# Kernel optimization log

Hardware: AMD Instinct MI355X
Metric: run time of the kernel (lower is better)

The kernel has to match this reference:

```python
import jax, jax.numpy as jnp
import numpy as np

N, E, IN, ED, HID, B, K = 50000, 800000, 128, 64, 256, 128, 1000


def setup_inputs() -> dict:
    key = jax.random.key(0)
    ks = jax.random.split(key, 16)

    def lin(k, fi, fo):
        k1, k2 = jax.random.split(k)
        s = 1.0 / np.sqrt(fi)
        return (jax.random.uniform(k1, (fi, fo), jnp.float32, -s, s),
                jax.random.uniform(k2, (fo,), jnp.float32, -s, s))

    We, be = lin(ks[0], ED, IN)        # GINEConv edge projection edge_dim -> in_channels
    W1, b1 = lin(ks[1], IN, HID)       # GINE nn layer 1
    W2, b2 = lin(ks[2], HID, HID)      # GINE nn layer 2
    Wg1, bg1 = lin(ks[3], HID, 128)    # gate_nn layer 1
    Wg2, bg2 = lin(ks[4], 128, 1)      # gate_nn layer 2
    Wh, bh = lin(ks[5], HID, K)        # head

    x = jax.random.normal(ks[6], (N, IN), jnp.float32)
    edge_index = jax.random.randint(ks[7], (2, E), 0, N, jnp.int64)
    edge_attr = jax.random.normal(ks[8], (E, ED), jnp.float32)
    batch = jnp.sort(jax.random.randint(ks[9], (N,), 0, B, jnp.int64))

    return {"x": x, "edge_index": edge_index, "edge_attr": edge_attr, "batch": batch,
            "We": We, "be": be, "W1": W1, "b1": b1, "W2": W2, "b2": b2,
            "Wg1": Wg1, "bg1": bg1, "Wg2": Wg2, "bg2": bg2, "Wh": Wh, "bh": bh}


def reference(x, edge_index, edge_attr, batch, We, be, W1, b1, W2, b2,
              Wg1, bg1, Wg2, bg2, Wh, bh):
    src, dst = edge_index[0], edge_index[1]
    # GINEConv message: ReLU(x_j + Lin(edge_attr)), scatter-add to dst (eps=0)
    e = edge_attr @ We + be                      # [E, IN]
    m = jax.nn.relu(x[src] + e)                  # [E, IN]
    agg = jax.ops.segment_sum(m, dst, num_segments=N)  # [N, IN]
    h = x + agg                                  # (1+eps)*x + agg, eps=0
    h = jax.nn.relu(h @ W1 + b1) @ W2 + b2       # [N, HID]
    # GlobalAttention: segment softmax of gate over graphs, weighted sum
    gate = jax.nn.relu(h @ Wg1 + bg1) @ Wg2 + bg2            # [N, 1]
    gmax = jax.ops.segment_max(gate, batch, num_segments=B)  # [B, 1]
    a = jnp.exp(gate - gmax[batch])
    denom = jax.ops.segment_sum(a, batch, num_segments=B)    # [B, 1]
    attn = a / denom[batch]
    pooled = jax.ops.segment_sum(attn * h, batch, num_segments=B)  # [B, HID]
    logits = pooled @ Wh + bh                    # [B, K]
    return (logits, pooled)
```

## Files before the change

kernel.cpp:

```cpp
#include <hip/hip_runtime.h>
#include <stdint.h>

#define NN    50000
#define EE    800000
#define IN_C  128
#define ED_C  64
#define HID_C 256
#define BB    128
#define KK    1000
#define G1_C  128
#define NV    50176


typedef __attribute__((ext_vector_type(8))) short bfrag;
typedef __attribute__((ext_vector_type(4))) float f4acc;

__device__ __forceinline__ unsigned short f2bs(float f){
  unsigned u = __float_as_uint(f);
  return (unsigned short)((u + 0x7fffu + ((u >> 16) & 1u)) >> 16);
}
__device__ __forceinline__ float bs2f(unsigned short s){
  return __uint_as_float(((unsigned)s) << 16);
}

__device__ __forceinline__ void atomicMaxFloat(float* addr, float val){
  int old = __float_as_int(*addr);
  while (__int_as_float(old) < val){
    int assumed = old;
    old = atomicCAS((int*)addr, assumed, __float_as_int(val));
    if (old == assumed) break;
  }
}

__global__ __launch_bounds__(256) void k_setup(
    const float* __restrict__ We, const float* __restrict__ W1,
    const float* __restrict__ W2, const float* __restrict__ Wg1,
    const float* __restrict__ x,
    unsigned short* __restrict__ Wet, unsigned short* __restrict__ W1t,
    unsigned short* __restrict__ W2t, unsigned short* __restrict__ Wg1t,
    unsigned short* __restrict__ xb,
    float* __restrict__ agg, int* __restrict__ cnt, int* __restrict__ fill,
    int* __restrict__ aux, float* __restrict__ gmax, float* __restrict__ denom,
    float* __restrict__ pooled)
{
  size_t i = (size_t)blockIdx.x * 256 + threadIdx.x;
  if (i < 128 * 64){ int c = (int)i >> 6, k = (int)i & 63;  Wet[i]  = f2bs(We[k * 128 + c]); }
  if (i < 256 * 128){ int n = (int)i >> 7, k = (int)i & 127; W1t[i]  = f2bs(W1[k * 256 + n]); }
  if (i < 256 * 256){ int n = (int)i >> 8, k = (int)i & 255; W2t[i]  = f2bs(W2[k * 256 + n]); }
  if (i < 128 * 256){ int n = (int)i >> 8, k = (int)i & 255; Wg1t[i] = f2bs(Wg1[k * 128 + n]); }
  if (i < (size_t)NN * IN_C / 4){
    const float4 v = ((const float4*)x)[i];
    ushort4 o;
    o.x = f2bs(v.x); o.y = f2bs(v.y); o.z = f2bs(v.z); o.w = f2bs(v.w);
    ((ushort4*)xb)[i] = o;
  }
  if (i < (size_t)NN * IN_C) agg[i] = 0.f;
  if (i < NV){ cnt[i] = 0; fill[i] = 0; }
  if (i < 256) aux[i] = 0;
  if (i < BB){ gmax[i] = -1e30f; denom[i] = 0.f; }
  if (i < BB * HID_C) pooled[i] = 0.f;
}

__global__ __launch_bounds__(256) void k_hist(const int* __restrict__ ei,
                                              int* __restrict__ cnt){
  int e = blockIdx.x * 256 + threadIdx.x;
  if (e < EE) atomicAdd(&cnt[ei[EE + e]], 1);
}

__global__ __launch_bounds__(256) void k_scan1(const int* __restrict__ cnt,
                                               int* __restrict__ off,
                                               int* __restrict__ aux){
  __shared__ int s[256];
  int t = threadIdx.x, i = blockIdx.x * 256 + t;
  int val = cnt[i];
  s[t] = val; __syncthreads();
#pragma unroll
  for (int o = 1; o < 256; o <<= 1){
    int v = (t >= o) ? s[t - o] : 0;
    __syncthreads();
    s[t] += v;
    __syncthreads();
  }
  off[i] = s[t] - val;
  if (t == 255) aux[blockIdx.x] = s[255];
}

__global__ __launch_bounds__(256) void k_scan2(int* __restrict__ aux){
  __shared__ int s[256];
  int t = threadIdx.x;
  int val = aux[t];
  s[t] = val; __syncthreads();
#pragma unroll
  for (int o = 1; o < 256; o <<= 1){
    int v = (t >= o) ? s[t - o] : 0;
    __syncthreads();
    s[t] += v;
    __syncthreads();
  }
  aux[t] = s[t] - val;
}

__global__ __launch_bounds__(256) void k_scan3(int* __restrict__ off,
                                               const int* __restrict__ aux){
  int i = blockIdx.x * 256 + threadIdx.x;
  off[i] += aux[blockIdx.x];
}

__global__ __launch_bounds__(256) void k_scatter(const int* __restrict__ ei,
                                                 const int* __restrict__ off,
                                                 int* __restrict__ fill,
                                                 uint4* __restrict__ sorted){
  int e = blockIdx.x * 256 + threadIdx.x;
  if (e < EE){
    int s = ei[e], d = ei[EE + e];
    int pos = off[d] + atomicAdd(&fill[d], 1);
    sorted[pos] = make_uint4((unsigned)e, (unsigned)s, (unsigned)d, 0u);
  }
}

__global__ __launch_bounds__(256, 4) void k_edge2(
    const unsigned short* __restrict__ xb, const uint4* __restrict__ sorted,
    const float* __restrict__ edge_attr,
    const unsigned short* __restrict__ Wet, const float* __restrict__ be,
    float* __restrict__ agg)
{
  __shared__ float msgS[64 * 132];
  __shared__ uint4 sE[64];
  __shared__ int runStart[66];
  __shared__ int nRunsS;
  unsigned short* eaS = (unsigned short*)msgS;

  const int tid = threadIdx.x;
  const int e0 = blockIdx.x * 64;
  if (tid < 64) sE[tid] = sorted[e0 + tid];
  __syncthreads();

  const int lane = tid & 63, wv = tid >> 6;
  const int q = lane >> 4, l15 = lane & 15;
  const int g0 = wv * 16;

  const int xrow = g0 + (lane >> 2);
  const int xc0 = (lane & 3) * 32;
  const unsigned short* xptr = xb + (size_t)((int)sE[xrow].y) * IN_C + xc0;
  uint4 xr[4];
#pragma unroll
  for (int j = 0; j < 4; ++j) xr[j] = *(const uint4*)(xptr + j * 8);

#pragma unroll
  for (int t = 0; t < 4; ++t){
    int f4 = t * 256 + tid;
    int er = f4 >> 4;
    int kk = (f4 & 15) * 4;
    int eid = (int)sE[er].x;
    const float4 v = *(const float4*)(edge_attr + (size_t)eid * ED_C + kk);
    unsigned p0 = (unsigned)f2bs(v.x) | ((unsigned)f2bs(v.y) << 16);
    unsigned p1 = (unsigned)f2bs(v.z) | ((unsigned)f2bs(v.w) << 16);
    *(uint2*)&eaS[er * 72 + kk] = make_uint2(p0, p1);
  }

  if (tid < 64){
    bool flag = (tid == 0) || ((int)sE[tid].z != (int)sE[tid - 1].z);
    unsigned long long m = __ballot(flag);
    int pre = __popcll(m & ((1ull << tid) - 1ull));
    if ((m >> tid) & 1ull) runStart[pre] = tid;
    if (tid == 0){
      int nr = __popcll(m);
      nRunsS = nr;
      runStart[nr] = 64;
    }
  }
  __syncthreads();

  f4acc acc[8];
  const f4acc zz = {0.f, 0.f, 0.f, 0.f};
#pragma unroll
  for (int nt = 0; nt < 8; ++nt) acc[nt] = zz;

#pragma unroll
  for (int ks = 0; ks < 2; ++ks){
    bfrag a = *(const bfrag*)&eaS[(g0 + l15) * 72 + ks * 32 + q * 8];
#pragma unroll
    for (int nt = 0; nt < 8; ++nt){
      int c = nt * 16 + l15;
      bfrag b = *(const bfrag*)(Wet + c * ED_C + ks * 32 + q * 8);
      acc[nt] = __builtin_amdgcn_mfma_f32_16x16x32_bf16(a, b, acc[nt], 0, 0, 0);
    }
  }

  float bev[8];
#pragma unroll
  for (int nt = 0; nt < 8; ++nt) bev[nt] = be[nt * 16 + l15];

  __syncthreads();

#pragma unroll
  for (int nt = 0; nt < 8; ++nt){
    int c = nt * 16 + l15;
#pragma unroll
    for (int r = 0; r < 4; ++r)
      msgS[(g0 + q * 4 + r) * 132 + c] = acc[nt][r] + bev[nt];
  }

  {
    float* mr = &msgS[xrow * 132 + xc0];
#pragma unroll
    for (int jj = 0; jj < 4; ++jj){
      const uint4 u = xr[jj];
      float4 w0 = *(float4*)(mr + jj * 8);
      float4 w1 = *(float4*)(mr + jj * 8 + 4);
      w0.x = fmaxf(w0.x + __uint_as_float(u.x << 16), 0.f);
      w0.y = fmaxf(w0.y + __uint_as_float(u.x & 0xffff0000u), 0.f);
      w0.z = fmaxf(w0.z + __uint_as_float(u.y << 16), 0.f);
      w0.w = fmaxf(w0.w + __uint_as_float(u.y & 0xffff0000u), 0.f);
      w1.x = fmaxf(w1.x + __uint_as_float(u.z << 16), 0.f);
      w1.y = fmaxf(w1.y + __uint_as_float(u.z & 0xffff0000u), 0.f);
      w1.z = fmaxf(w1.z + __uint_as_float(u.w << 16), 0.f);
      w1.w = fmaxf(w1.w + __uint_as_float(u.w & 0xffff0000u), 0.f);
      *(float4*)(mr + jj * 8) = w0;
      *(float4*)(mr + jj * 8 + 4) = w1;
    }
  }
  __syncthreads();

  {
    const int col = tid & 127;
    const int h = tid >> 7;
    const int nR = nRunsS;
    for (int i = h; i < nR; i += 2){
      int s = runStart[i], e = runStart[i + 1];
      int dst = (int)sE[s].z;
      float run = 0.f;
      for (int r = s; r < e; ++r) run += msgS[r * 132 + col];
      size_t a = (size_t)dst * IN_C + col;
      if (s == 0 || e == 64) atomicAdd(&agg[a], run);
      else                   agg[a] = run;
    }
  }
}

__global__ __launch_bounds__(256) void k_h0(const float* __restrict__ agg,
                                            const float* __restrict__ x,
                                            unsigned short* __restrict__ h0b){
  int i = blockIdx.x * 256 + threadIdx.x;
  if (i < NN * IN_C) h0b[i] = f2bs(agg[i] + x[i]);
}

template<int K, bool RELU, bool OB16, bool GATE>
__global__ __launch_bounds__(256) void k_gemm(
    const unsigned short* __restrict__ A, const unsigned short* __restrict__ Wt,
    const float* __restrict__ bias, unsigned short* __restrict__ outb,
    int M, int Ntot,
    const float* __restrict__ Wg2, const float* __restrict__ bg2,
    float* __restrict__ gateOut)
{
  __shared__ unsigned short aS[64 * 40];
  __shared__ unsigned short bS[128 * 40];
  __shared__ float gred[2][64];
  const int tid = threadIdx.x;
  const int lane = tid & 63, wv = tid >> 6;
  const int wi = wv >> 1, wj = wv & 1;
  const int q = lane >> 4, l15 = lane & 15;
  const int mb0 = blockIdx.x * 64;
  const int nb0 = blockIdx.y * 128;
  const int arow = tid >> 2, achk = tid & 3;

  f4acc acc[2][4];
  const f4acc zz = {0.f, 0.f, 0.f, 0.f};
#pragma unroll
  for (int mt = 0; mt < 2; ++mt)
#pragma unroll
    for (int nt = 0; nt < 4; ++nt) acc[mt][nt] = zz;

  for (int ks = 0; ks < K / 32; ++ks){
    {
      int m = mb0 + arow; if (m >= M) m = M - 1;
      const uint4 v = *(const uint4*)(A + (size_t)m * K + ks * 32 + achk * 8);
      *(uint4*)&aS[arow * 40 + achk * 8] = v;
    }
#pragma unroll
    for (int i = 0; i < 2; ++i){
      int idx = i * 256 + tid;
      int row = idx >> 2, chk = idx & 3;
      const uint4 v = *(const uint4*)(Wt + (size_t)(nb0 + row) * K + ks * 32 + chk * 8);
      *(uint4*)&bS[row * 40 + chk * 8] = v;
    }
    __syncthreads();
    bfrag a[2], b[4];
#pragma unroll
    for (int mt = 0; mt < 2; ++mt)
      a[mt] = *(const bfrag*)&aS[(wi * 32 + mt * 16 + l15) * 40 + q * 8];
#pragma unroll
    for (int nt = 0; nt < 4; ++nt)
      b[nt] = *(const bfrag*)&bS[(wj * 64 + nt * 16 + l15) * 40 + q * 8];
#pragma unroll
    for (int mt = 0; mt < 2; ++mt)
#pragma unroll
      for (int nt = 0; nt < 4; ++nt)
        acc[mt][nt] = __builtin_amdgcn_mfma_f32_16x16x32_bf16(a[mt], b[nt], acc[mt][nt], 0, 0, 0);
    __syncthreads();
  }

  const int mb = mb0 + wi * 32;
  const int nb = nb0 + wj * 64;

  if (GATE){
    float wg2v[4];
#pragma unroll
    for (int nt = 0; nt < 4; ++nt) wg2v[nt] = Wg2[wj * 64 + nt * 16 + l15];
    float pr[2][4];
#pragma unroll
    for (int mt = 0; mt < 2; ++mt)
#pragma unroll
      for (int r = 0; r < 4; ++r) pr[mt][r] = 0.f;
#pragma unroll
    for (int nt = 0; nt < 4; ++nt){
      float bv = bias[wj * 64 + nt * 16 + l15];
#pragma unroll
      for (int mt = 0; mt < 2; ++mt)
#pragma unroll
        for (int r = 0; r < 4; ++r){
          float v = acc[mt][nt][r] + bv;
          v = v > 0.f ? v : 0.f;
          pr[mt][r] = fmaf(v, wg2v[nt], pr[mt][r]);
        }
    }
#pragma unroll
    for (int off = 1; off < 16; off <<= 1)
#pragma unroll
      for (int mt = 0; mt < 2; ++mt)
#pragma unroll
        for (int r = 0; r < 4; ++r)
          pr[mt][r] += __shfl_xor(pr[mt][r], off);
    if (l15 == 0){
#pragma unroll
      for (int mt = 0; mt < 2; ++mt)
#pragma unroll
        for (int r = 0; r < 4; ++r)
          gred[wj][wi * 32 + mt * 16 + q * 4 + r] = pr[mt][r];
    }
    __syncthreads();
    if (tid < 64){
      int m = mb0 + tid;
      if (m < M) gateOut[m] = gred[0][tid] + gred[1][tid] + bg2[0];
    }
  } else {
#pragma unroll
    for (int nt = 0; nt < 4; ++nt){
      int c = nb + nt * 16 + l15;
      float bv = bias[c];
#pragma unroll
      for (int mt = 0; mt < 2; ++mt){
#pragma unroll
        for (int r = 0; r < 4; ++r){
          int m = mb + mt * 16 + q * 4 + r;
          if (m < M){
            float v = acc[mt][nt][r] + bv;
            if (RELU) v = v > 0.f ? v : 0.f;
            if (OB16) outb[(size_t)m * Ntot + c] = f2bs(v);
          }
        }
      }
    }
  }
}

__global__ __launch_bounds__(256) void k_gmax(const float* __restrict__ gate,
                                              const int* __restrict__ batch,
                                              float* __restrict__ gmax, int nrows){
  __shared__ float wred[4];
  const int tid = threadIdx.x;
  const int n0 = blockIdx.x * 256;
  const int n = n0 + tid;
  const int nlast = (n0 + 255 < nrows) ? n0 + 255 : nrows - 1;
  const int bmin = batch[n0], bmax = batch[nlast];
  const int lane = tid & 63, wv = tid >> 6;
  float val = -3e38f; int b = bmax;
  if (n < nrows){ b = batch[n]; val = gate[n]; }
  for (int bb = bmin; bb <= bmax; ++bb){
    float v = (b == bb) ? val : -3e38f;
#pragma unroll
    for (int off = 1; off < 64; off <<= 1) v = fmaxf(v, __shfl_xor(v, off));
    if (lane == 0) wred[wv] = v;
    __syncthreads();
    if (tid == 0){
      float m = fmaxf(fmaxf(wred[0], wred[1]), fmaxf(wred[2], wred[3]));
      if (m > -1e37f) atomicMaxFloat(&gmax[bb], m);
    }
    __syncthreads();
  }
}

__global__ __launch_bounds__(256) void k_expsum(const float* __restrict__ gate,
                                                const int* __restrict__ batch,
                                                const float* __restrict__ gmax,
                                                float* __restrict__ aexp,
                                                float* __restrict__ denom, int nrows){
  __shared__ float wred[4];
  const int tid = threadIdx.x;
  const int n0 = blockIdx.x * 256;
  const int n = n0 + tid;
  const int nlast = (n0 + 255 < nrows) ? n0 + 255 : nrows - 1;
  const int bmin = batch[n0], bmax = batch[nlast];
  const int lane = tid & 63, wv = tid >> 6;
  float val = 0.f; int b = bmax;
  if (n < nrows){
    b = batch[n];
    val = expf(gate[n] - gmax[b]);
    aexp[n] = val;
  }
  for (int bb = bmin; bb <= bmax; ++bb){
    float v = (b == bb) ? val : 0.f;
#pragma unroll
    for (int off = 1; off < 64; off <<= 1) v += __shfl_xor(v, off);
    if (lane == 0) wred[wv] = v;
    __syncthreads();
    if (tid == 0){
      float s = wred[0] + wred[1] + wred[2] + wred[3];
      if (s != 0.f) atomicAdd(&denom[bb], s);
    }
    __syncthreads();
  }
}

__global__ __launch_bounds__(256) void k_pool(const unsigned short* __restrict__ h2b,
                                              const float* __restrict__ aexp,
                                              const float* __restrict__ denom,
                                              const int* __restrict__ batch,
                                              float* __restrict__ pooled, int nrows){
  const int c = threadIdx.x;
  const int n0 = blockIdx.x * 32;
  int n1 = n0 + 32; if (n1 > nrows) n1 = nrows;
  if (n0 >= nrows) return;
  float acc = 0.f;
  int curb = batch[n0];
  for (int n = n0; n < n1; ++n){
    int b = batch[n];
    if (b != curb){
      atomicAdd(&pooled[(size_t)curb * HID_C + c], acc);
      acc = 0.f; curb = b;
    }
    float wgt = aexp[n] / denom[b];
    acc = fmaf(wgt, bs2f(h2b[(size_t)n * HID_C + c]), acc);
  }
  atomicAdd(&pooled[(size_t)curb * HID_C + c], acc);
}

__global__ __launch_bounds__(256) void k_head(const float* __restrict__ pooled,
                                              const float* __restrict__ Wh,
                                              const float* __restrict__ bh,
                                              float* __restrict__ out_logits,
                                              float* __restrict__ out_pooled){
  __shared__ float p[HID_C];
  const int b = blockIdx.x, t = threadIdx.x;
  float pv = pooled[(size_t)b * HID_C + t];
  p[t] = pv;
  out_pooled[(size_t)b * HID_C + t] = pv;
  __syncthreads();
  for (int c = t; c < KK; c += 256){
    float acc = bh[c];
#pragma unroll 8
    for (int k = 0; k < HID_C; ++k)
      acc = fmaf(p[k], Wh[k * KK + c], acc);
    out_logits[(size_t)b * KK + c] = acc;
  }
}

extern "C" void kernel_launch(void* const* d_in, const int* in_sizes, int n_in,
                              void* d_out, int out_size, void* d_ws, size_t ws_size,
                              hipStream_t stream) {
  const float* x   = (const float*)d_in[0];
  const int*   ei  = (const int*)d_in[1];
  const float* ea  = (const float*)d_in[2];
  const int*   batch = (const int*)d_in[3];
  const float* We  = (const float*)d_in[4];
  const float* be  = (const float*)d_in[5];
  const float* W1  = (const float*)d_in[6];
  const float* b1  = (const float*)d_in[7];
  const float* W2  = (const float*)d_in[8];
  const float* b2  = (const float*)d_in[9];
  const float* Wg1 = (const float*)d_in[10];
  const float* bg1 = (const float*)d_in[11];
  const float* Wg2 = (const float*)d_in[12];
  const float* bg2 = (const float*)d_in[13];
  const float* Wh  = (const float*)d_in[14];
  const float* bh  = (const float*)d_in[15];

  float* out_logits = (float*)d_out;
  float* out_pooled = out_logits + (size_t)BB * KK;

  float* agg    = (float*)d_ws;
  float* gate   = agg   + (size_t)NN * IN_C;
  float* aexp   = gate  + NN;
  float* gmax   = aexp  + NN;
  float* denom  = gmax  + BB;
  float* pooled = denom + BB;
  float* fend   = pooled + (size_t)BB * HID_C;
  unsigned short* h0b  = (unsigned short*)fend;
  unsigned short* h1b  = h0b + (size_t)NN * IN_C;
  unsigned short* h2b  = h1b + (size_t)NN * HID_C;
  unsigned short* Wet  = h2b + (size_t)NN * HID_C;
  unsigned short* W1t  = Wet + 128 * 64;
  unsigned short* W2t  = W1t + 256 * 128;
  unsigned short* Wg1t = W2t + 256 * 256;
  unsigned short* xb   = Wg1t + 128 * 256;
  uint4* sorted = (uint4*)h1b;
  int* cnt  = (int*)(sorted + EE);
  int* off  = cnt + NV;
  int* fill = off + NV;
  int* aux  = fill + NV;

  k_setup<<<(NN * IN_C + 255) / 256, 256, 0, stream>>>(
      We, W1, W2, Wg1, x, Wet, W1t, W2t, Wg1t, xb,
      agg, cnt, fill, aux, gmax, denom, pooled);
  k_hist   <<<(EE + 255) / 256, 256, 0, stream>>>(ei, cnt);
  k_scan1  <<<NV / 256, 256, 0, stream>>>(cnt, off, aux);
  k_scan2  <<<1, 256, 0, stream>>>(aux);
  k_scan3  <<<NV / 256, 256, 0, stream>>>(off, aux);
  k_scatter<<<(EE + 255) / 256, 256, 0, stream>>>(ei, off, fill, sorted);
  k_edge2<<<EE / 64, 256, 0, stream>>>(xb, sorted, ea, Wet, be, agg);
  k_h0<<<(NN * IN_C + 255) / 256, 256, 0, stream>>>(agg, x, h0b);
  k_gemm<128, true,  true,  false><<<dim3(782, 2), 256, 0, stream>>>(
      h0b, W1t, b1, h1b, NN, HID_C, (const float*)0, (const float*)0, (float*)0);
  k_gemm<256, false, true,  false><<<dim3(782, 2), 256, 0, stream>>>(
      h1b, W2t, b2, h2b, NN, HID_C, (const float*)0, (const float*)0, (float*)0);
  k_gemm<256, true,  false, true ><<<dim3(782, 1), 256, 0, stream>>>(
      h2b, Wg1t, bg1, (unsigned short*)0, NN, G1_C, Wg2, bg2, gate);
  k_gmax  <<<(NN + 255) / 256, 256, 0, stream>>>(gate, batch, gmax, NN);
  k_expsum<<<(NN + 255) / 256, 256, 0, stream>>>(gate, batch, gmax, aexp, denom, NN);
  k_pool  <<<(NN + 31) / 32, 256, 0, stream>>>(h2b, aexp, denom, batch, pooled, NN);
  k_head<<<BB, 256, 0, stream>>>(pooled, Wh, bh, out_logits, out_pooled);
}
```

Baseline: 666.9 us.

## Fuse h0 into first GEMM, merge attention pooling and head, trim scans

Removes the k_h0 pass by having the first GEMM load fp32 agg and x, add them and convert to bf16 while staging the A tile. Replaces the gmax/expsum/pool/head kernels with one kernel per graph that binary-searches its node range in the sorted batch array. That kernel computes max, softmax denominator, pooled features and logits with no global atomics. It also folds the scan3 pass into scatter by adding the block offset there, and reuses the cnt array as the fill counter by zeroing it inside scan1. The trade-off is that the fused attention stage runs on only 128 blocks, each walking about 390 nodes serially, and the first GEMM now reads fp32 A, which is twice as many bytes, for each N-tile.

```diff
diff --git a/kernel.cpp b/kernel.cpp
--- a/kernel.cpp
+++ b/kernel.cpp
@@ -23,15 +23,6 @@
   return __uint_as_float(((unsigned)s) << 16);
 }
 
-__device__ __forceinline__ void atomicMaxFloat(float* addr, float val){
-  int old = __float_as_int(*addr);
-  while (__int_as_float(old) < val){
-    int assumed = old;
-    old = atomicCAS((int*)addr, assumed, __float_as_int(val));
-    if (old == assumed) break;
-  }
-}
-
 __global__ __launch_bounds__(256) void k_setup(
     const float* __restrict__ We, const float* __restrict__ W1,
     const float* __restrict__ W2, const float* __restrict__ Wg1,
@@ -39,9 +30,7 @@
     unsigned short* __restrict__ Wet, unsigned short* __restrict__ W1t,
     unsigned short* __restrict__ W2t, unsigned short* __restrict__ Wg1t,
     unsigned short* __restrict__ xb,
-    float* __restrict__ agg, int* __restrict__ cnt, int* __restrict__ fill,
-    int* __restrict__ aux, float* __restrict__ gmax, float* __restrict__ denom,
-    float* __restrict__ pooled)
+    float* __restrict__ agg, int* __restrict__ cnt, int* __restrict__ aux)
 {
   size_t i = (size_t)blockIdx.x * 256 + threadIdx.x;
   if (i < 128 * 64){ int c = (int)i >> 6, k = (int)i & 63;  Wet[i]  = f2bs(We[k * 128 + c]); }
@@ -55,10 +44,8 @@
     ((ushort4*)xb)[i] = o;
   }
   if (i < (size_t)NN * IN_C) agg[i] = 0.f;
-  if (i < NV){ cnt[i] = 0; fill[i] = 0; }
+  if (i < NV) cnt[i] = 0;
   if (i < 256) aux[i] = 0;
-  if (i < BB){ gmax[i] = -1e30f; denom[i] = 0.f; }
-  if (i < BB * HID_C) pooled[i] = 0.f;
 }
 
 __global__ __launch_bounds__(256) void k_hist(const int* __restrict__ ei,
@@ -67,7 +54,7 @@
   if (e < EE) atomicAdd(&cnt[ei[EE + e]], 1);
 }
 
-__global__ __launch_bounds__(256) void k_scan1(const int* __restrict__ cnt,
+__global__ __launch_bounds__(256) void k_scan1(int* __restrict__ cnt,
                                                int* __restrict__ off,
                                                int* __restrict__ aux){
   __shared__ int s[256];
@@ -82,6 +69,7 @@
     __syncthreads();
   }
   off[i] = s[t] - val;
+  cnt[i] = 0;
   if (t == 255) aux[blockIdx.x] = s[255];
 }
 
@@ -100,20 +88,15 @@
   aux[t] = s[t] - val;
 }
 
-__global__ __launch_bounds__(256) void k_scan3(int* __restrict__ off,
-                                               const int* __restrict__ aux){
-  int i = blockIdx.x * 256 + threadIdx.x;
-  off[i] += aux[blockIdx.x];
-}
-
 __global__ __launch_bounds__(256) void k_scatter(const int* __restrict__ ei,
                                                  const int* __restrict__ off,
+                                                 const int* __restrict__ aux,
                                                  int* __restrict__ fill,
                                                  uint4* __restrict__ sorted){
   int e = blockIdx.x * 256 + threadIdx.x;
   if (e < EE){
     int s = ei[e], d = ei[EE + e];
-    int pos = off[d] + atomicAdd(&fill[d], 1);
+    int pos = off[d] + aux[d >> 8] + atomicAdd(&fill[d], 1);
     sorted[pos] = make_uint4((unsigned)e, (unsigned)s, (unsigned)d, 0u);
   }
 }
@@ -238,16 +221,11 @@
   }
 }
 
-__global__ __launch_bounds__(256) void k_h0(const float* __restrict__ agg,
-                                            const float* __restrict__ x,
-                                            unsigned short* __restrict__ h0b){
-  int i = blockIdx.x * 256 + threadIdx.x;
-  if (i < NN * IN_C) h0b[i] = f2bs(agg[i] + x[i]);
-}
-
-template<int K, bool RELU, bool OB16, bool GATE>
+template<int K, bool RELU, bool OB16, bool GATE, bool AF>
 __global__ __launch_bounds__(256) void k_gemm(
-    const unsigned short* __restrict__ A, const unsigned short* __restrict__ Wt,
+    const unsigned short* __restrict__ A,
+    const float* __restrict__ aggA, const float* __restrict__ xA,
+    const unsigned short* __restrict__ Wt,
     const float* __restrict__ bias, unsigned short* __restrict__ outb,
     int M, int Ntot,
     const float* __restrict__ Wg2, const float* __restrict__ bg2,
@@ -274,8 +252,23 @@
   for (int ks = 0; ks < K / 32; ++ks){
     {
       int m = mb0 + arow; if (m >= M) m = M - 1;
-      const uint4 v = *(const uint4*)(A + (size_t)m * K + ks * 32 + achk * 8);
-      *(uint4*)&aS[arow * 40 + achk * 8] = v;
+      if (AF){
+        size_t base = (size_t)m * K + ks * 32 + achk * 8;
+        const float4 a0 = *(const float4*)(aggA + base);
+        const float4 a1 = *(const float4*)(aggA + base + 4);
+        const float4 x0 = *(const float4*)(xA + base);
+        const float4 x1 = *(const float4*)(xA + base + 4);
+        ushort4 o0, o1;
+        o0.x = f2bs(a0.x + x0.x); o0.y = f2bs(a0.y + x0.y);
+        o0.z = f2bs(a0.z + x0.z); o0.w = f2bs(a0.w + x0.w);
+        o1.x = f2bs(a1.x + x1.x); o1.y = f2bs(a1.y + x1.y);
+        o1.z = f2bs(a1.z + x1.z); o1.w = f2bs(a1.w + x1.w);
+        *(ushort4*)&aS[arow * 40 + achk * 8] = o0;
+        *(ushort4*)&aS[arow * 40 + achk * 8 + 4] = o1;
+      } else {
+        const uint4 v = *(const uint4*)(A + (size_t)m * K + ks * 32 + achk * 8);
+        *(uint4*)&aS[arow * 40 + achk * 8] = v;
+      }
     }
 #pragma unroll
     for (int i = 0; i < 2; ++i){
@@ -364,104 +357,61 @@
   }
 }
 
-__global__ __launch_bounds__(256) void k_gmax(const float* __restrict__ gate,
-                                              const int* __restrict__ batch,
-                                              float* __restrict__ gmax, int nrows){
-  __shared__ float wred[4];
-  const int tid = threadIdx.x;
-  const int n0 = blockIdx.x * 256;
-  const int n = n0 + tid;
-  const int nlast = (n0 + 255 < nrows) ? n0 + 255 : nrows - 1;
-  const int bmin = batch[n0], bmax = batch[nlast];
-  const int lane = tid & 63, wv = tid >> 6;
-  float val = -3e38f; int b = bmax;
-  if (n < nrows){ b = batch[n]; val = gate[n]; }
-  for (int bb = bmin; bb <= bmax; ++bb){
-    float v = (b == bb) ? val : -3e38f;
-#pragma unroll
-    for (int off = 1; off < 64; off <<= 1) v = fmaxf(v, __shfl_xor(v, off));
-    if (lane == 0) wred[wv] = v;
-    __syncthreads();
-    if (tid == 0){
-      float m = fmaxf(fmaxf(wred[0], wred[1]), fmaxf(wred[2], wred[3]));
-      if (m > -1e37f) atomicMaxFloat(&gmax[bb], m);
-    }
-    __syncthreads();
-  }
-}
-
-__global__ __launch_bounds__(256) void k_expsum(const float* __restrict__ gate,
-                                                const int* __restrict__ batch,
-                                                const float* __restrict__ gmax,
-                                                float* __restrict__ aexp,
-                                                float* __restrict__ denom, int nrows){
-  __shared__ float wred[4];
-  const int tid = threadIdx.x;
-  const int n0 = blockIdx.x * 256;
-  const int n = n0 + tid;
-  const int nlast = (n0 + 255 < nrows) ? n0 + 255 : nrows - 1;
-  const int bmin = batch[n0], bmax = batch[nlast];
-  const int lane = tid & 63, wv = tid >> 6;
-  float val = 0.f; int b = bmax;
-  if (n < nrows){
-    b = batch[n];
-    val = expf(gate[n] - gmax[b]);
-    aexp[n] = val;
-  }
-  for (int bb = bmin; bb <= bmax; ++bb){
-    float v = (b == bb) ? val : 0.f;
-#pragma unroll
-    for (int off = 1; off < 64; off <<= 1) v += __shfl_xor(v, off);
-    if (lane == 0) wred[wv] = v;
-    __syncthreads();
-    if (tid == 0){
-      float s = wred[0] + wred[1] + wred[2] + wred[3];
-      if (s != 0.f) atomicAdd(&denom[bb], s);
-    }
-    __syncthreads();
-  }
-}
-
-__global__ __launch_bounds__(256) void k_pool(const unsigned short* __restrict__ h2b,
-                                              const float* __restrict__ aexp,
-                                              const float* __restrict__ denom,
-                                              const int* __restrict__ batch,
-                                              float* __restrict__ pooled, int nrows){
-  const int c = threadIdx.x;
-  const int n0 = blockIdx.x * 32;
-  int n1 = n0 + 32; if (n1 > nrows) n1 = nrows;
-  if (n0 >= nrows) return;
+__global__ __launch_bounds__(256) void k_attn(
+    const float* __restrict__ gate, const int* __restrict__ batch,
+    const unsigned short* __restrict__ h2b,
+    const float* __restrict__ Wh, const float* __restrict__ bh, int nrows,
+    float* __restrict__ out_logits, float* __restrict__ out_pooled)
+{
+  __shared__ float red[256];
+  __shared__ int seg[2];
+  __shared__ float pS[HID_C];
+  const int b = blockIdx.x, t = threadIdx.x;
+
+  if (t == 0){
+    int lo = 0, hi = nrows;
+    while (lo < hi){ int mid = (lo + hi) >> 1; if (batch[mid] < b) lo = mid + 1; else hi = mid; }
+    seg[0] = lo;
+    int lo2 = lo, hi2 = nrows;
+    while (lo2 < hi2){ int mid = (lo2 + hi2) >> 1; if (batch[mid] < b + 1) lo2 = mid + 1; else hi2 = mid; }
+    seg[1] = lo2;
+  }
+  __syncthreads();
+  const int lo = seg[0], hi = seg[1];
+
+  float m = -3e38f;
+  for (int n = lo + t; n < hi; n += 256) m = fmaxf(m, gate[n]);
+  red[t] = m; __syncthreads();
+  for (int s = 128; s > 0; s >>= 1){
+    if (t < s) red[t] = fmaxf(red[t], red[t + s]);
+    __syncthreads();
+  }
+  m = red[0]; __syncthreads();
+
+  float dsum = 0.f;
+  for (int n = lo + t; n < hi; n += 256) dsum += expf(gate[n] - m);
+  red[t] = dsum; __syncthreads();
+  for (int s = 128; s > 0; s >>= 1){
+    if (t < s) red[t] += red[t + s];
+    __syncthreads();
+  }
+  const float invd = (hi > lo) ? 1.f / red[0] : 0.f;
+
   float acc = 0.f;
-  int curb = batch[n0];
-  for (int n = n0; n < n1; ++n){
-    int b = batch[n];
-    if (b != curb){
-      atomicAdd(&pooled[(size_t)curb * HID_C + c], acc);
-      acc = 0.f; curb = b;
-    }
-    float wgt = aexp[n] / denom[b];
-    acc = fmaf(wgt, bs2f(h2b[(size_t)n * HID_C + c]), acc);
-  }
-  atomicAdd(&pooled[(size_t)curb * HID_C + c], acc);
-}
-
-__global__ __launch_bounds__(256) void k_head(const float* __restrict__ pooled,
-                                              const float* __restrict__ Wh,
-                                              const float* __restrict__ bh,
-                                              float* __restrict__ out_logits,
-                                              float* __restrict__ out_pooled){
-  __shared__ float p[HID_C];
-  const int b = blockIdx.x, t = threadIdx.x;
-  float pv = pooled[(size_t)b * HID_C + t];
-  p[t] = pv;
-  out_pooled[(size_t)b * HID_C + t] = pv;
-  __syncthreads();
+  for (int n = lo; n < hi; ++n){
+    float w = expf(gate[n] - m) * invd;
+    acc = fmaf(w, bs2f(h2b[(size_t)n * HID_C + t]), acc);
+  }
+  out_pooled[(size_t)b * HID_C + t] = acc;
+  pS[t] = acc;
+  __syncthreads();
+
   for (int c = t; c < KK; c += 256){
-    float acc = bh[c];
+    float a2 = bh[c];
 #pragma unroll 8
     for (int k = 0; k < HID_C; ++k)
-      acc = fmaf(p[k], Wh[k * KK + c], acc);
-    out_logits[(size_t)b * KK + c] = acc;
+      a2 = fmaf(pS[k], Wh[k * KK + c], a2);
+    out_logits[(size_t)b * KK + c] = a2;
   }
 }
 
@@ -488,15 +438,10 @@
   float* out_logits = (float*)d_out;
   float* out_pooled = out_logits + (size_t)BB * KK;
 
-  float* agg    = (float*)d_ws;
-  float* gate   = agg   + (size_t)NN * IN_C;
-  float* aexp   = gate  + NN;
-  float* gmax   = aexp  + NN;
-  float* denom  = gmax  + BB;
-  float* pooled = denom + BB;
-  float* fend   = pooled + (size_t)BB * HID_C;
-  unsigned short* h0b  = (unsigned short*)fend;
-  unsigned short* h1b  = h0b + (size_t)NN * IN_C;
+  float* agg  = (float*)d_ws;
+  float* gate = agg + (size_t)NN * IN_C;
+  float* fend = gate + NN;
+  unsigned short* h1b  = (unsigned short*)fend;
   unsigned short* h2b  = h1b + (size_t)NN * HID_C;
   unsigned short* Wet  = h2b + (size_t)NN * HID_C;
   unsigned short* W1t  = Wet + 128 * 64;
@@ -506,27 +451,24 @@
   uint4* sorted = (uint4*)h1b;
   int* cnt  = (int*)(sorted + EE);
   int* off  = cnt + NV;
-  int* fill = off + NV;
-  int* aux  = fill + NV;
+  int* aux  = off + NV;
 
   k_setup<<<(NN * IN_C + 255) / 256, 256, 0, stream>>>(
-      We, W1, W2, Wg1, x, Wet, W1t, W2t, Wg1t, xb,
-      agg, cnt, fill, aux, gmax, denom, pooled);
+      We, W1, W2, Wg1, x, Wet, W1t, W2t, Wg1t, xb, agg, cnt, aux);
   k_hist   <<<(EE + 255) / 256, 256, 0, stream>>>(ei, cnt);
   k_scan1  <<<NV / 256, 256, 0, stream>>>(cnt, off, aux);
   k_scan2  <<<1, 256, 0, stream>>>(aux);
-  k_scan3  <<<NV / 256, 256, 0, stream>>>(off, aux);
-  k_scatter<<<(EE + 255) / 256, 256, 0, stream>>>(ei, off, fill, sorted);
+  k_scatter<<<(EE + 255) / 256, 256, 0, stream>>>(ei, off, aux, cnt, sorted);
   k_edge2<<<EE / 64, 256, 0, stream>>>(xb, sorted, ea, Wet, be, agg);
-  k_h0<<<(NN * IN_C + 255) / 256, 256, 0, stream>>>(agg, x, h0b);
-  k_gemm<128, true,  true,  false><<<dim3(782, 2), 256, 0, stream>>>(
-      h0b, W1t, b1, h1b, NN, HID_C, (const float*)0, (const float*)0, (float*)0);
-  k_gemm<256, false, true,  false><<<dim3(782, 2), 256, 0, stream>>>(
-      h1b, W2t, b2, h2b, NN, HID_C, (const float*)0, (const float*)0, (float*)0);
-  k_gemm<256, true,  false, true ><<<dim3(782, 1), 256, 0, stream>>>(
-      h2b, Wg1t, bg1, (unsigned short*)0, NN, G1_C, Wg2, bg2, gate);
-  k_gmax  <<<(NN + 255) / 256, 256, 0, stream>>>(gate, batch, gmax, NN);
-  k_expsum<<<(NN + 255) / 256, 256, 0, stream>>>(gate, batch, gmax, aexp, denom, NN);
-  k_pool  <<<(NN + 31) / 32, 256, 0, stream>>>(h2b, aexp, denom, batch, pooled, NN);
-  k_head<<<BB, 256, 0, stream>>>(pooled, Wh, bh, out_logits, out_pooled);
-}
+  k_gemm<128, true,  true,  false, true ><<<dim3(782, 2), 256, 0, stream>>>(
+      (const unsigned short*)0, agg, x, W1t, b1, h1b, NN, HID_C,
+      (const float*)0, (const float*)0, (float*)0);
+  k_gemm<256, false, true,  false, false><<<dim3(782, 2), 256, 0, stream>>>(
+      h1b, (const float*)0, (const float*)0, W2t, b2, h2b, NN, HID_C,
+      (const float*)0, (const float*)0, (float*)0);
+  k_gemm<256, true,  false, true,  false><<<dim3(782, 1), 256, 0, stream>>>(
+      h2b, (const float*)0, (const float*)0, Wg1t, bg1, (unsigned short*)0, NN, G1_C,
+      Wg2, bg2, gate);
+  k_attn<<<BB, 256, 0, stream>>>(gate, batch, h2b, Wh, bh, NN,
+                                 out_logits, out_pooled);
+}
```

Measured after the change: 721.9 us. 1.08x slower.

## Make edge kernel persistent with prefetch pipelining and compact sorted edge records

Applied to the files above, without the earlier changes.

The edge-message kernel becomes a persistent grid of 512 blocks that loop over 64-edge tiles. The next tile's edge_attr and source x rows are prefetched into registers while the current tile is computed, and edge-projection weights are held in registers across tiles. Sorted edge records shrink from uint4 to uint2 by packing src and dst into 16 bits each, which relies on N being under 65536. The separate scan3 kernel is removed by adding the block offset inside scatter, and the count buffer is reused as the fill counter, which saves a launch and some memory traffic. The cost is higher register and LDS pressure (occupancy hint drops to 2) plus more complex barrier handling.

```diff
diff --git a/kernel.cpp b/kernel.cpp
--- a/kernel.cpp
+++ b/kernel.cpp
@@ -10,6 +10,7 @@
 #define KK    1000
 #define G1_C  128
 #define NV    50176
+#define EG    512
 
 
 typedef __attribute__((ext_vector_type(8))) short bfrag;
@@ -39,8 +40,8 @@
     unsigned short* __restrict__ Wet, unsigned short* __restrict__ W1t,
     unsigned short* __restrict__ W2t, unsigned short* __restrict__ Wg1t,
     unsigned short* __restrict__ xb,
-    float* __restrict__ agg, int* __restrict__ cnt, int* __restrict__ fill,
-    int* __restrict__ aux, float* __restrict__ gmax, float* __restrict__ denom,
+    float* __restrict__ agg, int* __restrict__ cnt, int* __restrict__ aux,
+    float* __restrict__ gmax, float* __restrict__ denom,
     float* __restrict__ pooled)
 {
   size_t i = (size_t)blockIdx.x * 256 + threadIdx.x;
@@ -55,7 +56,7 @@
     ((ushort4*)xb)[i] = o;
   }
   if (i < (size_t)NN * IN_C) agg[i] = 0.f;
-  if (i < NV){ cnt[i] = 0; fill[i] = 0; }
+  if (i < NV) cnt[i] = 0;
   if (i < 256) aux[i] = 0;
   if (i < BB){ gmax[i] = -1e30f; denom[i] = 0.f; }
   if (i < BB * HID_C) pooled[i] = 0.f;
@@ -67,7 +68,7 @@
   if (e < EE) atomicAdd(&cnt[ei[EE + e]], 1);
 }
 
-__global__ __launch_bounds__(256) void k_scan1(const int* __restrict__ cnt,
+__global__ __launch_bounds__(256) void k_scan1(int* __restrict__ cnt,
                                                int* __restrict__ off,
                                                int* __restrict__ aux){
   __shared__ int s[256];
@@ -82,6 +83,7 @@
     __syncthreads();
   }
   off[i] = s[t] - val;
+  cnt[i] = 0;
   if (t == 255) aux[blockIdx.x] = s[255];
 }
 
@@ -100,141 +102,195 @@
   aux[t] = s[t] - val;
 }
 
-__global__ __launch_bounds__(256) void k_scan3(int* __restrict__ off,
-                                               const int* __restrict__ aux){
-  int i = blockIdx.x * 256 + threadIdx.x;
-  off[i] += aux[blockIdx.x];
-}
-
 __global__ __launch_bounds__(256) void k_scatter(const int* __restrict__ ei,
                                                  const int* __restrict__ off,
+                                                 const int* __restrict__ aux,
                                                  int* __restrict__ fill,
-                                                 uint4* __restrict__ sorted){
+                                                 uint2* __restrict__ sorted){
   int e = blockIdx.x * 256 + threadIdx.x;
   if (e < EE){
     int s = ei[e], d = ei[EE + e];
-    int pos = off[d] + atomicAdd(&fill[d], 1);
-    sorted[pos] = make_uint4((unsigned)e, (unsigned)s, (unsigned)d, 0u);
-  }
-}
-
-__global__ __launch_bounds__(256, 4) void k_edge2(
-    const unsigned short* __restrict__ xb, const uint4* __restrict__ sorted,
+    int pos = off[d] + aux[d >> 8] + atomicAdd(&fill[d], 1);
+    sorted[pos] = make_uint2((unsigned)e, (unsigned)s | ((unsigned)d << 16));
+  }
+}
+
+__global__ __launch_bounds__(256, 2) void k_edge2(
+    const unsigned short* __restrict__ xb, const uint2* __restrict__ sorted,
     const float* __restrict__ edge_attr,
     const unsigned short* __restrict__ Wet, const float* __restrict__ be,
     float* __restrict__ agg)
 {
   __shared__ float msgS[64 * 132];
-  __shared__ uint4 sE[64];
-  __shared__ int runStart[66];
-  __shared__ int nRunsS;
-  unsigned short* eaS = (unsigned short*)msgS;
+  __shared__ uint2 sE[3][64];
+  __shared__ unsigned short eaS[2][64 * 72];
+  __shared__ int runStart[2][66];
+  __shared__ int nRunsS[2];
 
   const int tid = threadIdx.x;
-  const int e0 = blockIdx.x * 64;
-  if (tid < 64) sE[tid] = sorted[e0 + tid];
-  __syncthreads();
-
   const int lane = tid & 63, wv = tid >> 6;
   const int q = lane >> 4, l15 = lane & 15;
   const int g0 = wv * 16;
-
   const int xrow = g0 + (lane >> 2);
   const int xc0 = (lane & 3) * 32;
-  const unsigned short* xptr = xb + (size_t)((int)sE[xrow].y) * IN_C + xc0;
-  uint4 xr[4];
-#pragma unroll
-  for (int j = 0; j < 4; ++j) xr[j] = *(const uint4*)(xptr + j * 8);
-
-#pragma unroll
-  for (int t = 0; t < 4; ++t){
-    int f4 = t * 256 + tid;
-    int er = f4 >> 4;
-    int kk = (f4 & 15) * 4;
-    int eid = (int)sE[er].x;
-    const float4 v = *(const float4*)(edge_attr + (size_t)eid * ED_C + kk);
-    unsigned p0 = (unsigned)f2bs(v.x) | ((unsigned)f2bs(v.y) << 16);
-    unsigned p1 = (unsigned)f2bs(v.z) | ((unsigned)f2bs(v.w) << 16);
-    *(uint2*)&eaS[er * 72 + kk] = make_uint2(p0, p1);
-  }
+  const int NT = EE / 64;
+  const int t0 = blockIdx.x;
+
+  bfrag bW[2][8];
+#pragma unroll
+  for (int ks = 0; ks < 2; ++ks)
+#pragma unroll
+    for (int nt = 0; nt < 8; ++nt)
+      bW[ks][nt] = *(const bfrag*)(Wet + (size_t)(nt * 16 + l15) * ED_C + ks * 32 + q * 8);
+  float bev[8];
+#pragma unroll
+  for (int nt = 0; nt < 8; ++nt) bev[nt] = be[nt * 16 + l15];
 
   if (tid < 64){
-    bool flag = (tid == 0) || ((int)sE[tid].z != (int)sE[tid - 1].z);
-    unsigned long long m = __ballot(flag);
-    int pre = __popcll(m & ((1ull << tid) - 1ull));
-    if ((m >> tid) & 1ull) runStart[pre] = tid;
-    if (tid == 0){
-      int nr = __popcll(m);
-      nRunsS = nr;
-      runStart[nr] = 64;
-    }
+    sE[0][tid] = sorted[(size_t)t0 * 64 + tid];
+    if (t0 + EG < NT) sE[1][tid] = sorted[(size_t)(t0 + EG) * 64 + tid];
   }
   __syncthreads();
 
-  f4acc acc[8];
-  const f4acc zz = {0.f, 0.f, 0.f, 0.f};
-#pragma unroll
-  for (int nt = 0; nt < 8; ++nt) acc[nt] = zz;
-
-#pragma unroll
-  for (int ks = 0; ks < 2; ++ks){
-    bfrag a = *(const bfrag*)&eaS[(g0 + l15) * 72 + ks * 32 + q * 8];
+  uint4 xrA[4], xrB[4];
+  {
+#pragma unroll
+    for (int tt = 0; tt < 4; ++tt){
+      int f4 = tt * 256 + tid;
+      int er = f4 >> 4, kk = (f4 & 15) * 4;
+      int eid = (int)sE[0][er].x;
+      const float4 v = *(const float4*)(edge_attr + (size_t)eid * ED_C + kk);
+      unsigned p0 = (unsigned)f2bs(v.x) | ((unsigned)f2bs(v.y) << 16);
+      unsigned p1 = (unsigned)f2bs(v.z) | ((unsigned)f2bs(v.w) << 16);
+      *(uint2*)&eaS[0][er * 72 + kk] = make_uint2(p0, p1);
+    }
+    const unsigned short* xptr = xb + (size_t)(sE[0][xrow].y & 0xffffu) * IN_C + xc0;
+#pragma unroll
+    for (int j = 0; j < 4; ++j) xrA[j] = *(const uint4*)(xptr + j * 8);
+    if (tid < 64){
+      unsigned dc = sE[0][tid].y >> 16;
+      bool flag = (tid == 0) || (dc != (sE[0][tid - 1].y >> 16));
+      unsigned long long m = __ballot(flag);
+      int pre = __popcll(m & ((1ull << tid) - 1ull));
+      if ((m >> tid) & 1ull) runStart[0][pre] = tid;
+      if (tid == 0){ int nr = __popcll(m); nRunsS[0] = nr; runStart[0][nr] = 64; }
+    }
+  }
+  __syncthreads();
+
+  auto iterbody = [&](int i, int p, uint4 (&xrC)[4], uint4 (&xrN)[4]){
+    const int t = t0 + i * EG;
+    const int tn = t + EG, tnn = tn + EG;
+    const uint2* sEc = sE[i % 3];
+    const uint2* sEn = sE[(i + 1) % 3];
+    const bool hasN = tn < NT;
+
+    uint2 sereg = make_uint2(0u, 0u);
+    if (tid < 64 && tnn < NT) sereg = sorted[(size_t)tnn * 64 + tid];
+
+    float4 eL[4];
+    if (hasN){
+#pragma unroll
+      for (int tt = 0; tt < 4; ++tt){
+        int f4 = tt * 256 + tid;
+        int er = f4 >> 4, kk = (f4 & 15) * 4;
+        int eid = (int)sEn[er].x;
+        eL[tt] = *(const float4*)(edge_attr + (size_t)eid * ED_C + kk);
+      }
+      const unsigned short* xptr = xb + (size_t)(sEn[xrow].y & 0xffffu) * IN_C + xc0;
+#pragma unroll
+      for (int j = 0; j < 4; ++j) xrN[j] = *(const uint4*)(xptr + j * 8);
+    }
+
+    f4acc acc[8];
+    const f4acc zz = {0.f, 0.f, 0.f, 0.f};
+#pragma unroll
+    for (int nt = 0; nt < 8; ++nt) acc[nt] = zz;
+#pragma unroll
+    for (int ks = 0; ks < 2; ++ks){
+      bfrag a = *(const bfrag*)&eaS[p][(g0 + l15) * 72 + ks * 32 + q * 8];
+#pragma unroll
+      for (int nt = 0; nt < 8; ++nt)
+        acc[nt] = __builtin_amdgcn_mfma_f32_16x16x32_bf16(a, bW[ks][nt], acc[nt], 0, 0, 0);
+    }
 #pragma unroll
     for (int nt = 0; nt < 8; ++nt){
       int c = nt * 16 + l15;
-      bfrag b = *(const bfrag*)(Wet + c * ED_C + ks * 32 + q * 8);
-      acc[nt] = __builtin_amdgcn_mfma_f32_16x16x32_bf16(a, b, acc[nt], 0, 0, 0);
-    }
-  }
-
-  float bev[8];
-#pragma unroll
-  for (int nt = 0; nt < 8; ++nt) bev[nt] = be[nt * 16 + l15];
-
-  __syncthreads();
-
-#pragma unroll
-  for (int nt = 0; nt < 8; ++nt){
-    int c = nt * 16 + l15;
-#pragma unroll
-    for (int r = 0; r < 4; ++r)
-      msgS[(g0 + q * 4 + r) * 132 + c] = acc[nt][r] + bev[nt];
-  }
-
-  {
-    float* mr = &msgS[xrow * 132 + xc0];
-#pragma unroll
-    for (int jj = 0; jj < 4; ++jj){
-      const uint4 u = xr[jj];
-      float4 w0 = *(float4*)(mr + jj * 8);
-      float4 w1 = *(float4*)(mr + jj * 8 + 4);
-      w0.x = fmaxf(w0.x + __uint_as_float(u.x << 16), 0.f);
-      w0.y = fmaxf(w0.y + __uint_as_float(u.x & 0xffff0000u), 0.f);
-      w0.z = fmaxf(w0.z + __uint_as_float(u.y << 16), 0.f);
-      w0.w = fmaxf(w0.w + __uint_as_float(u.y & 0xffff0000u), 0.f);
-      w1.x = fmaxf(w1.x + __uint_as_float(u.z << 16), 0.f);
-      w1.y = fmaxf(w1.y + __uint_as_float(u.z & 0xffff0000u), 0.f);
-      w1.z = fmaxf(w1.z + __uint_as_float(u.w << 16), 0.f);
-      w1.w = fmaxf(w1.w + __uint_as_float(u.w & 0xffff0000u), 0.f);
-      *(float4*)(mr + jj * 8) = w0;
-      *(float4*)(mr + jj * 8 + 4) = w1;
-    }
-  }
-  __syncthreads();
-
-  {
-    const int col = tid & 127;
-    const int h = tid >> 7;
-    const int nR = nRunsS;
-    for (int i = h; i < nR; i += 2){
-      int s = runStart[i], e = runStart[i + 1];
-      int dst = (int)sE[s].z;
-      float run = 0.f;
-      for (int r = s; r < e; ++r) run += msgS[r * 132 + col];
-      size_t a = (size_t)dst * IN_C + col;
-      if (s == 0 || e == 64) atomicAdd(&agg[a], run);
-      else                   agg[a] = run;
-    }
+#pragma unroll
+      for (int r = 0; r < 4; ++r)
+        msgS[(g0 + q * 4 + r) * 132 + c] = acc[nt][r] + bev[nt];
+    }
+    {
+      float* mr = &msgS[xrow * 132 + xc0];
+#pragma unroll
+      for (int jj = 0; jj < 4; ++jj){
+        const uint4 u = xrC[jj];
+        float4 w0 = *(float4*)(mr + jj * 8);
+        float4 w1 = *(float4*)(mr + jj * 8 + 4);
+        w0.x = fmaxf(w0.x + __uint_as_float(u.x << 16), 0.f);
+        w0.y = fmaxf(w0.y + __uint_as_float(u.x & 0xffff0000u), 0.f);
+        w0.z = fmaxf(w0.z + __uint_as_float(u.y << 16), 0.f);
+        w0.w = fmaxf(w0.w + __uint_as_float(u.y & 0xffff0000u), 0.f);
+        w1.x = fmaxf(w1.x + __uint_as_float(u.z << 16), 0.f);
+        w1.y = fmaxf(w1.y + __uint_as_float(u.z & 0xffff0000u), 0.f);
+        w1.z = fmaxf(w1.z + __uint_as_float(u.w << 16), 0.f);
+        w1.w = fmaxf(w1.w + __uint_as_float(u.w & 0xffff0000u), 0.f);
+        *(float4*)(mr + jj * 8) = w0;
+        *(float4*)(mr + jj * 8 + 4) = w1;
+      }
+    }
+    asm volatile("s_waitcnt lgkmcnt(0)" ::: "memory");
+    __builtin_amdgcn_s_barrier();
+    __builtin_amdgcn_sched_barrier(0);
+
+    {
+      const int col = tid & 127;
+      const int h = tid >> 7;
+      const int nR = nRunsS[p];
+      for (int i2 = h; i2 < nR; i2 += 2){
+        int s = runStart[p][i2], e = runStart[p][i2 + 1];
+        int dst = (int)(sEc[s].y >> 16);
+        float run = 0.f;
+        for (int r = s; r < e; ++r) run += msgS[r * 132 + col];
+        size_t a = (size_t)dst * IN_C + col;
+        if (s == 0 || e == 64) atomicAdd(&agg[a], run);
+        else                   agg[a] = run;
+      }
+    }
+
+    if (hasN){
+#pragma unroll
+      for (int tt = 0; tt < 4; ++tt){
+        int f4 = tt * 256 + tid;
+        int er = f4 >> 4, kk = (f4 & 15) * 4;
+        unsigned p0 = (unsigned)f2bs(eL[tt].x) | ((unsigned)f2bs(eL[tt].y) << 16);
+        unsigned p1 = (unsigned)f2bs(eL[tt].z) | ((unsigned)f2bs(eL[tt].w) << 16);
+        *(uint2*)&eaS[p ^ 1][er * 72 + kk] = make_uint2(p0, p1);
+      }
+      if (tid < 64){
+        unsigned dc = sEn[tid].y >> 16;
+        bool flag = (tid == 0) || (dc != (sEn[tid - 1].y >> 16));
+        unsigned long long m = __ballot(flag);
+        int pre = __popcll(m & ((1ull << tid) - 1ull));
+        if ((m >> tid) & 1ull) runStart[p ^ 1][pre] = tid;
+        if (tid == 0){ int nr = __popcll(m); nRunsS[p ^ 1] = nr; runStart[p ^ 1][nr] = 64; }
+      }
+    }
+    if (tid < 64 && tnn < NT) sE[(i + 2) % 3][tid] = sereg;
+
+    asm volatile("s_waitcnt lgkmcnt(0)" ::: "memory");
+    __builtin_amdgcn_s_barrier();
+    __builtin_amdgcn_sched_barrier(0);
+  };
+
+  int i = 0;
+  for (;;){
+    if (t0 + i * EG >= NT) break;
+    iterbody(i, 0, xrA, xrB);
+    ++i;
+    if (t0 + i * EG >= NT) break;
+    iterbody(i, 1, xrB, xrA);
+    ++i;
   }
 }
 
@@ -503,21 +559,19 @@
   unsigned short* W2t  = W1t + 256 * 128;
   unsigned short* Wg1t = W2t + 256 * 256;
   unsigned short* xb   = Wg1t + 128 * 256;
-  uint4* sorted = (uint4*)h1b;
+  uint2* sorted = (uint2*)h1b;
   int* cnt  = (int*)(sorted + EE);
   int* off  = cnt + NV;
-  int* fill = off + NV;
-  int* aux  = fill + NV;
+  int* aux  = off + NV;
 
   k_setup<<<(NN * IN_C + 255) / 256, 256, 0, stream>>>(
       We, W1, W2, Wg1, x, Wet, W1t, W2t, Wg1t, xb,
-      agg, cnt, fill, aux, gmax, denom, pooled);
+      agg, cnt, aux, gmax, denom, pooled);
   k_hist   <<<(EE + 255) / 256, 256, 0, stream>>>(ei, cnt);
   k_scan1  <<<NV / 256, 256, 0, stream>>>(cnt, off, aux);
   k_scan2  <<<1, 256, 0, stream>>>(aux);
-  k_scan3  <<<NV / 256, 256, 0, stream>>>(off, aux);
-  k_scatter<<<(EE + 255) / 256, 256, 0, stream>>>(ei, off, fill, sorted);
-  k_edge2<<<EE / 64, 256, 0, stream>>>(xb, sorted, ea, Wet, be, agg);
+  k_scatter<<<(EE + 255) / 256, 256, 0, stream>>>(ei, off, aux, cnt, sorted);
+  k_edge2<<<EG, 256, 0, stream>>>(xb, sorted, ea, Wet, be, agg);
   k_h0<<<(NN * IN_C + 255) / 256, 256, 0, stream>>>(agg, x, h0b);
   k_gemm<128, true,  true,  false><<<dim3(782, 2), 256, 0, stream>>>(
       h0b, W1t, b1, h1b, NN, HID_C, (const float*)0, (const float*)0, (float*)0);
```

Result: faster. 634.3 us (-4.9%).
